# Kernel tuning notes

Measured on AMD Instinct MI355X. Metric: run time of the kernel, lower is better.

## Reference

```python
import jax, jax.numpy as jnp
import numpy as np

F_DIM = 64; HID = 256; P_ETA = 32; NBINS = 16; MULT = 3 * NBINS - 1
NLAYERS = 8; NBLOCKS = 2; TAIL = 10.0
MIN_BW = 1e-8; MIN_BH = 1e-8; MIN_D = 1e-8
THETA_DIM = F_DIM + 1
N_BATCH = 8192; M_DATA = 256


def _masks():
    in_deg = np.arange(1, F_DIM + 1)
    hid_deg = np.arange(HID) % (F_DIM - 1) + 1
    out_deg = np.repeat(in_deg, MULT)  # output index f*MULT+m has degree f+1
    m_in = (hid_deg[:, None] >= in_deg[None, :]).astype(np.float32)
    m_hh = (hid_deg[:, None] >= hid_deg[None, :]).astype(np.float32)
    m_out = (out_deg[:, None] > hid_deg[None, :]).astype(np.float32)
    return jnp.asarray(m_in), jnp.asarray(m_hh), jnp.asarray(m_out)


def _rqs_forward(x, uw, uh, ud):
    # unconstrained rational-quadratic spline with linear tails (nflows math)
    const = float(np.log(np.exp(1.0 - MIN_D) - 1.0))
    inside = (x >= -TAIL) & (x <= TAIL)
    ud = jnp.pad(ud, ((0, 0), (0, 0), (1, 1)), constant_values=const)  # [N,F,NBINS+1]
    w = jax.nn.softmax(uw, -1)
    w = MIN_BW + (1.0 - MIN_BW * NBINS) * w
    cw = jnp.concatenate([jnp.zeros_like(w[..., :1]), jnp.cumsum(w, -1)], -1)
    cw = 2.0 * TAIL * cw - TAIL
    cw = cw.at[..., 0].set(-TAIL).at[..., -1].set(TAIL)
    w = jnp.diff(cw, axis=-1)
    h = jax.nn.softmax(uh, -1)
    h = MIN_BH + (1.0 - MIN_BH * NBINS) * h
    ch = jnp.concatenate([jnp.zeros_like(h[..., :1]), jnp.cumsum(h, -1)], -1)
    ch = 2.0 * TAIL * ch - TAIL
    ch = ch.at[..., 0].set(-TAIL).at[..., -1].set(TAIL)
    h = jnp.diff(ch, axis=-1)
    d = MIN_D + jax.nn.softplus(ud)
    xs = jnp.clip(x, -TAIL, TAIL)
    idx = jnp.clip(jnp.sum((xs[..., None] >= cw).astype(jnp.int32), -1) - 1, 0, NBINS - 1)
    g = lambda a, i: jnp.take_along_axis(a, i[..., None], -1)[..., 0]
    icw, ich = g(cw, idx), g(ch, idx)
    iw, ih = g(w, idx), g(h, idx)
    delta = ih / iw
    d0, d1 = g(d, idx), g(d, idx + 1)
    t = (xs - icw) / iw
    tt = t * (1.0 - t)
    denom = delta + (d0 + d1 - 2.0 * delta) * tt
    y = ich + ih * (delta * t * t + d0 * tt) / denom
    dnum = delta * delta * (d1 * t * t + 2.0 * delta * tt + d0 * (1.0 - t) * (1.0 - t))
    ld = jnp.log(dnum) - 2.0 * jnp.log(denom)
    return jnp.where(inside, y, x), jnp.where(inside, ld, 0.0)


def _flow_transform(z, eta, W_in, b_in, W_ctx, b_ctx, W_blk, b_blk, W_out, b_out):
    m_in, m_hh, m_out = _masks()
    sqrt_h = jnp.sqrt(jnp.asarray(HID, z.dtype))

    def layer(carry, p):
        x, ld = carry
        Wi, bi, Wc, bc, Wb, bb, Wo, bo = p
        x = jnp.flip(x, axis=1)  # ReversePermutation (logdet 0)
        h = x @ (Wi * m_in).T + bi + eta @ Wc.T + bc  # MADE initial + context
        for k in range(NBLOCKS):  # masked pre-activation residual blocks
            t = jax.nn.relu(h)
            t = t @ (Wb[k, 0] * m_hh).T + bb[k, 0]
            t = jax.nn.relu(t)
            t = t @ (Wb[k, 1] * m_hh).T + bb[k, 1]
            h = h + t
        out = (h @ (Wo * m_out).T + bo).reshape(x.shape[0], F_DIM, MULT)
        uw = out[..., :NBINS] / sqrt_h
        uh = out[..., NBINS:2 * NBINS] / sqrt_h
        ud = out[..., 2 * NBINS:]
        x, l = _rqs_forward(x, uw, uh, ud)
        return (x, ld + l.sum(-1)), None

    init = (z, jnp.zeros(z.shape[0], z.dtype))
    (x, ld), _ = jax.lax.scan(layer, init, (W_in, b_in, W_ctx, b_ctx, W_blk, b_blk, W_out, b_out))
    return x, ld


def _stick_breaking(x):
    log_v = -jax.nn.softplus(-x)
    log_1v = -jax.nn.softplus(x)
    prefix = jnp.concatenate([jnp.zeros_like(x[:, :1]), jnp.cumsum(log_1v[:, :-1], 1)], 1)
    log_theta = jnp.concatenate([log_v + prefix, log_1v.sum(1, keepdims=True)], 1)
    wts = jnp.arange(F_DIM, 0, -1, dtype=x.dtype)
    log_det = log_v.sum(1) + (wts * log_1v).sum(1)
    return jnp.exp(log_theta), log_det


def setup_inputs() -> dict:
    key = jax.random.key(0)
    ks = jax.random.split(key, 8)
    s = 0.05
    return {
        'z': jax.random.normal(ks[0], (N_BATCH, F_DIM), jnp.float32),
        'eta_batch': jax.random.normal(ks[1], (N_BATCH, P_ETA), jnp.float32),
        'data_D2': jax.random.normal(ks[2], (M_DATA, THETA_DIM), jnp.float32),
        'W_in': s * jax.random.normal(ks[3], (NLAYERS, HID, F_DIM), jnp.float32),
        'b_in': jnp.zeros((NLAYERS, HID), jnp.float32),
        'W_ctx': s * jax.random.normal(ks[4], (NLAYERS, HID, P_ETA), jnp.float32),
        'b_ctx': jnp.zeros((NLAYERS, HID), jnp.float32),
        'W_blk': s * jax.random.normal(ks[5], (NLAYERS, NBLOCKS, 2, HID, HID), jnp.float32),
        'b_blk': jnp.zeros((NLAYERS, NBLOCKS, 2, HID), jnp.float32),
        'W_out': s * jax.random.normal(ks[6], (NLAYERS, F_DIM * MULT, HID), jnp.float32),
        'b_out': jnp.zeros((NLAYERS, F_DIM * MULT), jnp.float32),
    }


def reference(z, eta_batch, data_D2, W_in, b_in, W_ctx, b_ctx, W_blk, b_blk, W_out, b_out):
    x, flow_ld = _flow_transform(z, eta_batch, W_in, b_in, W_ctx, b_ctx, W_blk, b_blk, W_out, b_out)
    theta, sb_ld = _stick_breaking(x)
    total_ld = flow_ld + sb_ld
    log_qz = -0.5 * jnp.sum(z * z, -1) - 0.5 * F_DIM * jnp.log(2.0 * jnp.pi).astype(z.dtype)
    log_q = log_qz - total_ld
    # prior: Dirichlet(alpha=2) unnormalized: sum log(theta)
    log_p = jnp.sum(jnp.log(jnp.clip(theta, 1e-10, None)), -1)
    # likelihood: mean over data rows of isotropic Gaussian centered at theta
    d_sq = jnp.mean(jnp.sum(data_D2 * data_D2, -1))
    d_mean = jnp.mean(data_D2, 0)
    log_lik = -0.5 * (d_sq - 2.0 * theta @ d_mean + jnp.sum(theta * theta, -1))
    return jnp.mean(log_q - (log_p + log_lik))
```

## Files before the change

### kernel.cpp

```cpp
#include <hip/hip_runtime.h>
#include <hip/hip_fp8.h>
#include <math.h>

typedef float f32x4 __attribute__((ext_vector_type(4)));
typedef unsigned short u16;
typedef unsigned char u8;

typedef const __attribute__((address_space(1))) unsigned int ga_u32;
typedef __attribute__((address_space(3))) unsigned int ls_u32;

__device__ __forceinline__ void gl16(const void* g, void* l) {
    __builtin_amdgcn_global_load_lds((ga_u32*)g, (ls_u32*)l, 16, 0, 0);
}

__device__ __forceinline__ u16 f2bf(float f) {
    union { float f; unsigned u; } v; v.f = f;
    return (u16)((v.u + 0x7FFFu + ((v.u >> 16) & 1u)) >> 16);
}
__device__ __forceinline__ float bf2f(u16 h) {
    union { unsigned u; float f; } v; v.u = ((unsigned)h) << 16;
    return v.f;
}
__device__ __forceinline__ u8 f2q(float f) {
    __hip_fp8_e4m3 t(f);
    return (u8)t.__x;
}
__device__ __forceinline__ long ld8(const u8* p) { return *(const long*)p; }

__device__ __forceinline__ float splusf(float x) {
    return fmaxf(x, 0.f) + __logf(1.f + __expf(-fabsf(x)));
}
__device__ __forceinline__ int invperm(int k) {
    int m, q;
    if (k < 20) { m = k / 5; q = k - 5 * m; }
    else        { m = (k - 4) >> 2; q = (k - 4) & 3; }
    return m + 63 * q;
}

#define MID_ACT_P 272
#define WSCALE 64.f
#define WINV (1.f / 64.f)

__global__ __launch_bounds__(256) void setup_w(
    const float* __restrict__ Win, const float* __restrict__ bin,
    const float* __restrict__ Wctx, const float* __restrict__ bctx,
    const float* __restrict__ Wblk, const float* __restrict__ Wout,
    const float* __restrict__ bout, const float* __restrict__ eta,
    const float* __restrict__ z, const float* __restrict__ bblk,
    u8* __restrict__ W1, float* __restrict__ B1, u8* __restrict__ WB,
    u8* __restrict__ WO, float* __restrict__ BO, u8* __restrict__ AXE,
    float* __restrict__ XF, float* __restrict__ BBp)
{
    const long N1 = 8L * 8 * 8 * 64 * 8;
    const long N2 = 8L * 256;
    const long N3 = 8L * 4 * 8 * 9 * 64 * 8;
    const long N4 = 8L * 32 * 8 * 6 * 64 * 8;
    const long N5 = 8L * 3072;
    const long N6 = 8192L * 32;
    const long N7 = 8192L * 64;
    const long N8 = 8L * 4 * 256;
    const long tot = N1 + N2 + N3 + N4 + N5 + N6 + N7 + N8;
    for (long i = (long)blockIdx.x * blockDim.x + threadIdx.x; i < tot;
         i += (long)gridDim.x * blockDim.x) {
        long t = i;
        if (t < N1) {
            int off = (int)(t & 7), lane = (int)((t >> 3) & 63);
            int frag = (int)((t >> 9) & 7), wv = (int)((t >> 12) & 7);
            long l = t >> 15;
            int ks = frag >> 1, f = frag & 1;
            int pblk = f ? (15 - wv) : wv;
            int prow = pblk * 16 + (lane & 15);
            int row = invperm(prow);
            int c = ks * 32 + ((lane >> 4) << 3) + off;
            float v = 0.f;
            if (c < 64)      v = Win[(l * 256 + row) * 64 + c] * (((row % 63) >= c) ? 1.f : 0.f);
            else if (c < 96) v = Wctx[(l * 256 + row) * 32 + (c - 64)];
            W1[t] = f2q(v * WSCALE);
        } else if ((t -= N1) < N2) {
            long l = t >> 8; int k = (int)(t & 255);
            int c = invperm(k);
            B1[t] = bin[l * 256 + c] + bctx[l * 256 + c];
        } else if ((t -= N2) < N3) {
            int off = (int)(t & 7), lane = (int)((t >> 3) & 63);
            long r5 = t >> 9;
            int frag = (int)(r5 % 9); long r6 = r5 / 9;
            int wv = (int)(r6 & 7);
            int bi = (int)((r6 >> 3) & 3);
            long l = r6 >> 5;
            int kA = (wv + 2) >> 1;
            int pblk, ksl;
            if (frag < kA) { pblk = wv;      ksl = frag; }
            else           { pblk = 15 - wv; ksl = frag - kA; }
            int prow = pblk * 16 + (lane & 15);
            int pc   = ksl * 32 + ((lane >> 4) << 3) + off;
            int row = invperm(prow), c = invperm(pc);
            float v = Wblk[(((size_t)l * 4 + bi) * 256 + row) * 256 + c] *
                      (((row % 63) >= (c % 63)) ? 1.f : 0.f);
            WB[t] = f2q(v * WSCALE);
        } else if ((t -= N3) < N4) {
            long l = t / 786432; int rem = (int)(t % 786432);
            int y = rem / 24576, r2 = rem % 24576;
            int ks = r2 / 3072, r3 = r2 % 3072;
            int frag = r3 / 512, r4 = r3 % 512;
            int lane = r4 / 8, off = r4 % 8;
            int op = y * 96 + frag * 16 + (lane & 15);
            int pj = ks * 32 + ((lane >> 4) << 3) + off;
            int j = invperm(pj);
            int fd = op / 48, mm = op % 48;
            float v = 0.f;
            if (mm < 47 && fd > (j % 63))
                v = Wout[((size_t)l * 3008 + fd * 47 + mm) * 256 + j];
            WO[t] = f2q(v * WSCALE);
        } else if ((t -= N4) < N5) {
            long l = t / 3072; int op = (int)(t % 3072);
            int fd = op / 48, mm = op % 48;
            BO[t] = (mm < 47) ? bout[l * 3008 + (long)fd * 47 + mm] : 0.f;
        } else if ((t -= N5) < N6) {
            long b = t / 32; int p = (int)(t % 32);
            AXE[b * 96 + 64 + p] = f2q(eta[t]);
        } else if ((t -= N6) < N7) {
            long b = t >> 6; int f = (int)(t & 63);
            float v = z[b * 64 + (63 - f)];
            XF[t] = v;
            AXE[b * 96 + f] = f2q(v);
        } else {
            t -= N7;
            int k = (int)(t & 255);
            BBp[t] = bblk[(t & ~(long)255) | invperm(k)];
        }
    }
}

__global__ __launch_bounds__(128) void dstat(const float* __restrict__ D,
                                             float* __restrict__ DM)
{
    int j = threadIdx.x;
    float s = 0.f, q = 0.f;
    if (j < 65) {
        for (int m = 0; m < 256; ++m) {
            float v = D[m * 65 + j];
            s += v; q += v * v;
        }
        DM[j] = s * (1.f / 256.f);
    }
    __shared__ float red[128];
    red[j] = q; __syncthreads();
    for (int st = 64; st > 0; st >>= 1) {
        if (j < st) red[j] += red[j + st];
        __syncthreads();
    }
    if (j == 0) DM[65] = red[0] * (1.f / 256.f);
}

template<int KA>
__device__ __forceinline__ void wb_stage(
    const u8* __restrict__ gW, const u8* __restrict__ act,
    int lane, int fr, int kg, f32x4& T0, f32x4& T1)
{
    constexpr int KB = 9 - KA;
    long wf[9];
#pragma unroll
    for (int j = 0; j < 9; ++j)
        wf[j] = ld8(gW + (j * 64 + lane) * 8);
#pragma unroll
    for (int j = 0; j < KA; ++j) {
        long af = ld8(&act[fr * MID_ACT_P + j * 32 + kg * 8]);
        T0 = __builtin_amdgcn_mfma_f32_16x16x32_fp8_fp8(wf[j], af, T0, 0, 0, 0);
    }
#pragma unroll
    for (int j = 0; j < KB; ++j) {
        long af = ld8(&act[fr * MID_ACT_P + j * 32 + kg * 8]);
        T1 = __builtin_amdgcn_mfma_f32_16x16x32_fp8_fp8(wf[KA + j], af, T1, 0, 0, 0);
    }
}

__global__ __launch_bounds__(512) void fused_mid(
    const u8* __restrict__ AXE, const u8* __restrict__ W1l,
    const float* __restrict__ B1l, const u8* __restrict__ WBl,
    const float* __restrict__ bbl, u8* __restrict__ HB)
{
    __shared__ u8 act[2][16 * MID_ACT_P];
    const int tid = threadIdx.x;
    const int lane = tid & 63;
    const int wv = tid >> 6;
    const int fr = lane & 15, kg = lane >> 4;
    const int b0 = blockIdx.x * 16;
    const int cbA = wv * 16 + kg * 4;
    const int cbB = (15 - wv) * 16 + kg * 4;

    if (tid < 96) {
        int row = tid / 6, part = tid - row * 6;
        *(int4*)&act[0][row * MID_ACT_P + part * 16] =
            *(const int4*)&AXE[(size_t)(b0 + row) * 96 + part * 16];
    }

    f32x4 H0, H1, T0, T1;

    auto zeroT = [&]() {
        T0 = (f32x4){0.f, 0.f, 0.f, 0.f};
        T1 = (f32x4){0.f, 0.f, 0.f, 0.f};
    };
    auto epi1 = [&](f32x4& T, f32x4& H, int cb, const float* bias, int mode,
                    u8* actw) {
        const float4 bs = *(const float4*)&bias[cb];
        f32x4 v = T;
        v[0] = v[0] * WINV + bs.x; v[1] = v[1] * WINV + bs.y;
        v[2] = v[2] * WINV + bs.z; v[3] = v[3] * WINV + bs.w;
        if (mode == 0) H = v;
        if (mode == 2 || mode == 3) {
            H[0] += v[0]; H[1] += v[1]; H[2] += v[2]; H[3] += v[3];
            v = H;
        }
        unsigned pk;
        if (mode != 3) {
            pk = (unsigned)f2q(fmaxf(v[0], 0.f))
               | ((unsigned)f2q(fmaxf(v[1], 0.f)) << 8)
               | ((unsigned)f2q(fmaxf(v[2], 0.f)) << 16)
               | ((unsigned)f2q(fmaxf(v[3], 0.f)) << 24);
            *(unsigned*)&actw[fr * MID_ACT_P + cb] = pk;
        } else {
            pk = (unsigned)f2q(v[0]) | ((unsigned)f2q(v[1]) << 8)
               | ((unsigned)f2q(v[2]) << 16) | ((unsigned)f2q(v[3]) << 24);
            const int b = b0 + fr;
            const size_t idx =
                (((((size_t)(b >> 7) * 8 + (cb >> 5)) * 8 + ((b >> 4) & 7)) * 64)
                 + (((cb >> 3) & 3) * 16 + (b & 15))) * 8 + (cb & 7);
            *(unsigned*)&HB[idx] = pk;
        }
    };
    auto epi = [&](const float* bias, int mode, u8* actw) {
        epi1(T0, H0, cbA, bias, mode, actw);
        epi1(T1, H1, cbB, bias, mode, actw);
    };
    auto wbrun = [&](const u8* gW, const u8* actr) {
        switch (wv >> 1) {
        case 0: wb_stage<1>(gW, actr, lane, fr, kg, T0, T1); break;
        case 1: wb_stage<2>(gW, actr, lane, fr, kg, T0, T1); break;
        case 2: wb_stage<3>(gW, actr, lane, fr, kg, T0, T1); break;
        default: wb_stage<4>(gW, actr, lane, fr, kg, T0, T1); break;
        }
    };

    zeroT();
    {
        const u8* gW = W1l + wv * 4096;
        long wf[6];
#pragma unroll
        for (int j = 0; j < 6; ++j)
            wf[j] = ld8(gW + (j * 64 + lane) * 8);
        __syncthreads();
#pragma unroll
        for (int ks = 0; ks < 3; ++ks) {
            long af = ld8(&act[0][fr * MID_ACT_P + ks * 32 + kg * 8]);
            T0 = __builtin_amdgcn_mfma_f32_16x16x32_fp8_fp8(wf[ks * 2 + 0], af, T0, 0, 0, 0);
            T1 = __builtin_amdgcn_mfma_f32_16x16x32_fp8_fp8(wf[ks * 2 + 1], af, T1, 0, 0, 0);
        }
    }
    epi(B1l, 0, act[1]);
    zeroT();
    __syncthreads();
    wbrun(WBl + 0 * 36864 + wv * 4608, act[1]);
    epi(bbl, 1, act[0]);
    zeroT();
    __syncthreads();
    wbrun(WBl + 1 * 36864 + wv * 4608, act[0]);
    epi(bbl + 256, 2, act[1]);
    zeroT();
    __syncthreads();
    wbrun(WBl + 2 * 36864 + wv * 4608, act[1]);
    epi(bbl + 2 * 256, 1, act[0]);
    zeroT();
    __syncthreads();
    wbrun(WBl + 3 * 36864 + wv * 4608, act[0]);
    epi(bbl + 3 * 256, 3, (u8*)nullptr);
}

__global__ __launch_bounds__(256) void gemm_out_spline(
    const u8* __restrict__ A, const u8* __restrict__ Wo,
    const float* __restrict__ bo, const float* __restrict__ XF,
    float* __restrict__ Xn, float* __restrict__ XFnext, u8* __restrict__ AXE,
    float* __restrict__ LDP, int first)
{
    __shared__ u16 SM16[13312];
    u8* SM8 = (u8*)SM16;
    const int tid = threadIdx.x;
    const int lane = tid & 63, wv = tid >> 6;
    const int wm = wv >> 1, wn = wv & 1;
    const int fr = lane & 15, kg = lane >> 4;
    const int by = 31 - (int)blockIdx.y;
    const int m0 = blockIdx.x * 128, n0 = by * 96;
    const int nk = (by + 4) >> 2;

    u8* Ab = SM8;
    u8* Bb = SM8 + 8192;

    const u8* gA = A  + (size_t)blockIdx.x * 16384;
    const u8* gB = Wo + (size_t)by * 24576;

    f32x4 acc[4][3];
#pragma unroll
    for (int m = 0; m < 4; ++m)
#pragma unroll
        for (int n = 0; n < 3; ++n) acc[m][n] = (f32x4){0.f, 0.f, 0.f, 0.f};

    gl16(gA + tid * 16, Ab + tid * 16);
    if (tid < 192) gl16(gB + tid * 16, Bb + tid * 16);

    for (int ks = 0; ks < nk; ++ks) {
        __syncthreads();
        if (ks + 1 < nk) {
            const u8* sa = gA + (ks + 1) * 4096;
            const u8* sb = gB + (ks + 1) * 3072;
            u8* na = Ab + ((ks + 1) & 1) * 4096;
            u8* nb = Bb + ((ks + 1) & 1) * 3072;
            gl16(sa + tid * 16, na + tid * 16);
            if (tid < 192) gl16(sb + tid * 16, nb + tid * 16);
        }
        const u8* cA = Ab + (ks & 1) * 4096;
        const u8* cB = Bb + (ks & 1) * 3072;
        long af[4], bf[3];
#pragma unroll
        for (int m = 0; m < 4; ++m)
            af[m] = ld8(&cA[(wm * 4 + m) * 512 + lane * 8]);
#pragma unroll
        for (int n = 0; n < 3; ++n)
            bf[n] = ld8(&cB[(wn * 3 + n) * 512 + lane * 8]);
#pragma unroll
        for (int m = 0; m < 4; ++m)
#pragma unroll
            for (int n = 0; n < 3; ++n)
                acc[m][n] = __builtin_amdgcn_mfma_f32_16x16x32_fp8_fp8(bf[n], af[m], acc[m][n], 0, 0, 0);
    }
    __syncthreads();

#pragma unroll
    for (int m = 0; m < 4; ++m) {
        const int row = wm * 64 + m * 16 + fr;
#pragma unroll
        for (int n = 0; n < 3; ++n) {
            const int c0 = wn * 48 + n * 16 + kg * 4;
            const float4 bs = *(const float4*)&bo[n0 + c0];
            short4 q;
            q.x = (short)f2bf(acc[m][n][0] * WINV + bs.x);
            q.y = (short)f2bf(acc[m][n][1] * WINV + bs.y);
            q.z = (short)f2bf(acc[m][n][2] * WINV + bs.z);
            q.w = (short)f2bf(acc[m][n][3] * WINV + bs.w);
            *(short4*)&SM16[row * 104 + c0] = q;
        }
    }
    __syncthreads();

    typedef short bf16x8 __attribute__((ext_vector_type(8)));
    const int r = tid >> 1, fi = tid & 1;
    const int b = m0 + r;
    const int fg = by * 2 + fi;
    const u16* o_ = &SM16[r * 104 + fi * 48];
    bf16x8 v0 = *(const bf16x8*)(o_);
    bf16x8 v1 = *(const bf16x8*)(o_ + 8);
    bf16x8 v2 = *(const bf16x8*)(o_ + 16);
    bf16x8 v3 = *(const bf16x8*)(o_ + 24);
    bf16x8 v4 = *(const bf16x8*)(o_ + 32);
    bf16x8 v5 = *(const bf16x8*)(o_ + 40);

    float xin = XF[(size_t)b * 64 + fg];
    bool inside = (xin >= -10.f) && (xin <= 10.f);
    float xs = fminf(fmaxf(xin, -10.f), 10.f);

    float ew[16], eh[16], ud[15];
#pragma unroll
    for (int i = 0; i < 8; ++i) {
        ew[i]     = bf2f((u16)v0[i]) * 0.0625f;
        ew[8 + i] = bf2f((u16)v1[i]) * 0.0625f;
        eh[i]     = bf2f((u16)v2[i]) * 0.0625f;
        eh[8 + i] = bf2f((u16)v3[i]) * 0.0625f;
    }
#pragma unroll
    for (int i = 0; i < 8; ++i) ud[i] = bf2f((u16)v4[i]);
#pragma unroll
    for (int i = 0; i < 7; ++i) ud[8 + i] = bf2f((u16)v5[i]);

    float mw = ew[0], mh = eh[0];
#pragma unroll
    for (int i = 1; i < 16; ++i) { mw = fmaxf(mw, ew[i]); mh = fmaxf(mh, eh[i]); }
    float sw = 0.f, sh = 0.f;
#pragma unroll
    for (int i = 0; i < 16; ++i) {
        ew[i] = __expf(ew[i] - mw); sw += ew[i];
        eh[i] = __expf(eh[i] - mh); sh += eh[i];
    }
    const float kw = 20.f * (1.f - 1.6e-7f) / sw;
    const float kh = 20.f * (1.f - 1.6e-7f) / sh;

    float cwk = -10.f, chk = -10.f;
    float icw = -10.f, ich = -10.f, iw = 1.f, ih = 1.f, udl = 0.f, udr = 0.f;
    int selk = 0;
#pragma unroll
    for (int k = 0; k < 16; ++k) {
        const float cw1 = (k == 15) ? 10.f : cwk + (2e-7f + kw * ew[k]);
        const float ch1 = (k == 15) ? 10.f : chk + (2e-7f + kh * eh[k]);
        if (xs >= cwk) {
            selk = k;
            icw = cwk; iw = cw1 - cwk;
            ich = chk; ih = ch1 - chk;
            udl = (k >= 1)  ? ud[k - 1] : 0.f;
            udr = (k <= 14) ? ud[k]     : 0.f;
        }
        cwk = cw1; chk = ch1;
    }
    float d0 = (selk == 0)  ? 1.f : 1e-8f + splusf(udl);
    float d1 = (selk == 15) ? 1.f : 1e-8f + splusf(udr);
    float delta = ih / iw;
    float t = (xs - icw) / iw;
    float tt = t * (1.f - t);
    float denom = delta + (d0 + d1 - 2.f * delta) * tt;
    float y = ich + ih * (delta * t * t + d0 * tt) / denom;
    float omt = 1.f - t;
    float dnum = delta * delta * (d1 * t * t + 2.f * delta * tt + d0 * omt * omt);
    float ldv = __logf(dnum) - 2.f * __logf(denom);
    if (!inside) { y = xin; ldv = 0.f; }

    Xn[(size_t)b * 64 + fg] = y;
    XFnext[(size_t)b * 64 + (63 - fg)] = y;
    AXE[(size_t)b * 96 + (63 - fg)] = f2q(y);

    float other = __shfl_xor(ldv, 1);
    if (fi == 0) {
        size_t o = (size_t)b * 32 + by;
        float v = ldv + other;
        LDP[o] = first ? v : (LDP[o] + v);
    }
}

__global__ __launch_bounds__(256) void final1(
    const float* __restrict__ X, const float* __restrict__ z,
    const float* __restrict__ LDP, const float* __restrict__ DM,
    float* __restrict__ PART)
{
    int tid = threadIdx.x;
    int b = blockIdx.x * 256 + tid;
    float ldt = 0.f;
    for (int g = 0; g < 32; ++g) ldt += LDP[(size_t)b * 32 + g];
    float pre = 0.f, lvs = 0.f, wls = 0.f, lp = 0.f, tdm = 0.f, tsq = 0.f;
    const float LCLIP = -23.02585093f;
    for (int i = 0; i < 64; ++i) {
        float xi = X[(size_t)b * 64 + i];
        float lv = -splusf(-xi), l1 = -splusf(xi);
        float lt = lv + pre;
        float th = __expf(lt);
        lp += fmaxf(lt, LCLIP);
        tdm += th * DM[i]; tsq += th * th;
        lvs += lv; wls += (float)(64 - i) * l1;
        pre += l1;
    }
    float th = __expf(pre);
    lp += fmaxf(pre, LCLIP); tdm += th * DM[64]; tsq += th * th;
    float zs = 0.f;
    for (int i = 0; i < 64; ++i) { float zz = z[(size_t)b * 64 + i]; zs += zz * zz; }
    float logqz = -0.5f * zs - 58.812066f;
    float log_q = logqz - (ldt + lvs + wls);
    float log_lik = -0.5f * (DM[65] - 2.f * tdm + tsq);
    float val = log_q - lp - log_lik;

    __shared__ float red[256];
    red[tid] = val; __syncthreads();
    for (int s = 128; s > 0; s >>= 1) {
        if (tid < s) red[tid] += red[tid + s];
        __syncthreads();
    }
    if (tid == 0) PART[blockIdx.x] = red[0];
}

__global__ __launch_bounds__(64) void final2(const float* __restrict__ PART,
                                             float* __restrict__ out)
{
    int tid = threadIdx.x;
    float s = (tid < 32) ? PART[tid] : 0.f;
    for (int o = 16; o > 0; o >>= 1) s += __shfl_down(s, o);
    if (tid == 0) out[0] = s * (1.f / 8192.f);
}

extern "C" void kernel_launch(void* const* d_in, const int* in_sizes, int n_in,
                              void* d_out, int out_size, void* d_ws, size_t ws_size,
                              hipStream_t stream)
{
    (void)in_sizes; (void)n_in; (void)out_size; (void)ws_size;
    const float* z    = (const float*)d_in[0];
    const float* eta  = (const float*)d_in[1];
    const float* dat  = (const float*)d_in[2];
    const float* Win  = (const float*)d_in[3];
    const float* bin  = (const float*)d_in[4];
    const float* Wctx = (const float*)d_in[5];
    const float* bctx = (const float*)d_in[6];
    const float* Wblk = (const float*)d_in[7];
    const float* bblk = (const float*)d_in[8];
    const float* Wout = (const float*)d_in[9];
    const float* bout = (const float*)d_in[10];
    float* out = (float*)d_out;

    char* w = (char*)d_ws;
    size_t off = 0;
    auto alloc = [&](size_t bytes) {
        void* p = w + off;
        off += (bytes + 255) & ~(size_t)255;
        return p;
    };
    u8*    W1  = (u8*)   alloc(8L * 32768);
    float* B1  = (float*)alloc(8L * 256 * 4);
    u8*    WB  = (u8*)   alloc(8L * 147456);
    float* BBp = (float*)alloc(8L * 4 * 256 * 4);
    u8*    WO  = (u8*)   alloc(8L * 786432);
    float* BO  = (float*)alloc(8L * 3072 * 4);
    u8*    AXE = (u8*)   alloc(8192L * 96);
    float* XFa = (float*)alloc(8192L * 64 * 4);
    float* XFb = (float*)alloc(8192L * 64 * 4);
    float* XC  = (float*)alloc(8192L * 64 * 4);
    u8*    HB  = (u8*)   alloc(8192L * 256);
    float* LDP = (float*)alloc(8192L * 32 * 4);
    float* DM  = (float*)alloc(66 * 4);
    float* PART= (float*)alloc(64 * 4);

    setup_w<<<dim3(2048), dim3(256), 0, stream>>>(
        Win, bin, Wctx, bctx, Wblk, Wout, bout, eta, z, bblk,
        W1, B1, WB, WO, BO, AXE, XFa, BBp);
    dstat<<<dim3(1), dim3(128), 0, stream>>>(dat, DM);

    for (int l = 0; l < 8; ++l) {
        float* XFin  = (l & 1) ? XFb : XFa;
        float* XFout = (l & 1) ? XFa : XFb;
        fused_mid<<<dim3(512), dim3(512), 0, stream>>>(
            AXE, W1 + (size_t)l * 32768, B1 + l * 256,
            WB + (size_t)l * 147456, BBp + (size_t)l * 4 * 256, HB);
        gemm_out_spline<<<dim3(64, 32), dim3(256), 0, stream>>>(
            HB, WO + (size_t)l * 786432, BO + l * 3072, XFin,
            XC, XFout, AXE, LDP, (l == 0) ? 1 : 0);
    }
    final1<<<dim3(32), dim3(256), 0, stream>>>(XC, z, LDP, DM, PART);
    final2<<<dim3(1), dim3(64), 0, stream>>>(PART, out);
}
```

Measured before the change: 282.6 us.

## Pair complementary output tiles per block and fold data stats into final kernel

The output GEMM+spline kernel now runs half as many blocks, each processing two column tiles (by=31-p and by=p) whose K-depths are complementary, balancing the triangular MADE workload across blocks and reusing the A tile region. Separately, the single-block data-statistics kernel is removed and each final1 block recomputes the data means in shared memory, saving one launch at the cost of redundant reads of the small data matrix. Pairing reduces grid parallelism to 1024 blocks and serializes two tiles within each block.

```diff
diff --git a/kernel.cpp b/kernel.cpp
--- a/kernel.cpp
+++ b/kernel.cpp
@@ -131,27 +131,6 @@
     }
 }
 
-__global__ __launch_bounds__(128) void dstat(const float* __restrict__ D,
-                                             float* __restrict__ DM)
-{
-    int j = threadIdx.x;
-    float s = 0.f, q = 0.f;
-    if (j < 65) {
-        for (int m = 0; m < 256; ++m) {
-            float v = D[m * 65 + j];
-            s += v; q += v * v;
-        }
-        DM[j] = s * (1.f / 256.f);
-    }
-    __shared__ float red[128];
-    red[j] = q; __syncthreads();
-    for (int st = 64; st > 0; st >>= 1) {
-        if (j < st) red[j] += red[j + st];
-        __syncthreads();
-    }
-    if (j == 0) DM[65] = red[0] * (1.f / 256.f);
-}
-
 template<int KA>
 __device__ __forceinline__ void wb_stage(
     const u8* __restrict__ gW, const u8* __restrict__ act,
@@ -287,156 +266,185 @@
     const int lane = tid & 63, wv = tid >> 6;
     const int wm = wv >> 1, wn = wv & 1;
     const int fr = lane & 15, kg = lane >> 4;
-    const int by = 31 - (int)blockIdx.y;
-    const int m0 = blockIdx.x * 128, n0 = by * 96;
-    const int nk = (by + 4) >> 2;
+    const int p = (int)blockIdx.y;
+    const int m0 = blockIdx.x * 128;
 
     u8* Ab = SM8;
     u8* Bb = SM8 + 8192;
-
-    const u8* gA = A  + (size_t)blockIdx.x * 16384;
-    const u8* gB = Wo + (size_t)by * 24576;
-
-    f32x4 acc[4][3];
-#pragma unroll
-    for (int m = 0; m < 4; ++m)
-#pragma unroll
-        for (int n = 0; n < 3; ++n) acc[m][n] = (f32x4){0.f, 0.f, 0.f, 0.f};
-
-    gl16(gA + tid * 16, Ab + tid * 16);
-    if (tid < 192) gl16(gB + tid * 16, Bb + tid * 16);
-
-    for (int ks = 0; ks < nk; ++ks) {
+    const u8* gA = A + (size_t)blockIdx.x * 16384;
+
+    typedef short bf16x8 __attribute__((ext_vector_type(8)));
+
+#pragma unroll
+    for (int half = 0; half < 2; ++half) {
+        const int by = half ? p : (31 - p);
+        const int n0 = by * 96;
+        const int nk = (by + 4) >> 2;
+        const u8* gB = Wo + (size_t)by * 24576;
+
+        f32x4 acc[4][3];
+#pragma unroll
+        for (int m = 0; m < 4; ++m)
+#pragma unroll
+            for (int n = 0; n < 3; ++n) acc[m][n] = (f32x4){0.f, 0.f, 0.f, 0.f};
+
+        if (half) __syncthreads();
+
+        gl16(gA + tid * 16, Ab + tid * 16);
+        if (tid < 192) gl16(gB + tid * 16, Bb + tid * 16);
+
+        for (int ks = 0; ks < nk; ++ks) {
+            __syncthreads();
+            if (ks + 1 < nk) {
+                const u8* sa = gA + (ks + 1) * 4096;
+                const u8* sb = gB + (ks + 1) * 3072;
+                u8* na = Ab + ((ks + 1) & 1) * 4096;
+                u8* nb = Bb + ((ks + 1) & 1) * 3072;
+                gl16(sa + tid * 16, na + tid * 16);
+                if (tid < 192) gl16(sb + tid * 16, nb + tid * 16);
+            }
+            const u8* cA = Ab + (ks & 1) * 4096;
+            const u8* cB = Bb + (ks & 1) * 3072;
+            long af[4], bf[3];
+#pragma unroll
+            for (int m = 0; m < 4; ++m)
+                af[m] = ld8(&cA[(wm * 4 + m) * 512 + lane * 8]);
+#pragma unroll
+            for (int n = 0; n < 3; ++n)
+                bf[n] = ld8(&cB[(wn * 3 + n) * 512 + lane * 8]);
+#pragma unroll
+            for (int m = 0; m < 4; ++m)
+#pragma unroll
+                for (int n = 0; n < 3; ++n)
+                    acc[m][n] = __builtin_amdgcn_mfma_f32_16x16x32_fp8_fp8(bf[n], af[m], acc[m][n], 0, 0, 0);
+        }
         __syncthreads();
-        if (ks + 1 < nk) {
-            const u8* sa = gA + (ks + 1) * 4096;
-            const u8* sb = gB + (ks + 1) * 3072;
-            u8* na = Ab + ((ks + 1) & 1) * 4096;
-            u8* nb = Bb + ((ks + 1) & 1) * 3072;
-            gl16(sa + tid * 16, na + tid * 16);
-            if (tid < 192) gl16(sb + tid * 16, nb + tid * 16);
-        }
-        const u8* cA = Ab + (ks & 1) * 4096;
-        const u8* cB = Bb + (ks & 1) * 3072;
-        long af[4], bf[3];
-#pragma unroll
-        for (int m = 0; m < 4; ++m)
-            af[m] = ld8(&cA[(wm * 4 + m) * 512 + lane * 8]);
-#pragma unroll
-        for (int n = 0; n < 3; ++n)
-            bf[n] = ld8(&cB[(wn * 3 + n) * 512 + lane * 8]);
-#pragma unroll
-        for (int m = 0; m < 4; ++m)
-#pragma unroll
-            for (int n = 0; n < 3; ++n)
-                acc[m][n] = __builtin_amdgcn_mfma_f32_16x16x32_fp8_fp8(bf[n], af[m], acc[m][n], 0, 0, 0);
-    }
-    __syncthreads();
-
-#pragma unroll
-    for (int m = 0; m < 4; ++m) {
-        const int row = wm * 64 + m * 16 + fr;
-#pragma unroll
-        for (int n = 0; n < 3; ++n) {
-            const int c0 = wn * 48 + n * 16 + kg * 4;
-            const float4 bs = *(const float4*)&bo[n0 + c0];
-            short4 q;
-            q.x = (short)f2bf(acc[m][n][0] * WINV + bs.x);
-            q.y = (short)f2bf(acc[m][n][1] * WINV + bs.y);
-            q.z = (short)f2bf(acc[m][n][2] * WINV + bs.z);
-            q.w = (short)f2bf(acc[m][n][3] * WINV + bs.w);
-            *(short4*)&SM16[row * 104 + c0] = q;
-        }
-    }
-    __syncthreads();
-
-    typedef short bf16x8 __attribute__((ext_vector_type(8)));
-    const int r = tid >> 1, fi = tid & 1;
-    const int b = m0 + r;
-    const int fg = by * 2 + fi;
-    const u16* o_ = &SM16[r * 104 + fi * 48];
-    bf16x8 v0 = *(const bf16x8*)(o_);
-    bf16x8 v1 = *(const bf16x8*)(o_ + 8);
-    bf16x8 v2 = *(const bf16x8*)(o_ + 16);
-    bf16x8 v3 = *(const bf16x8*)(o_ + 24);
-    bf16x8 v4 = *(const bf16x8*)(o_ + 32);
-    bf16x8 v5 = *(const bf16x8*)(o_ + 40);
-
-    float xin = XF[(size_t)b * 64 + fg];
-    bool inside = (xin >= -10.f) && (xin <= 10.f);
-    float xs = fminf(fmaxf(xin, -10.f), 10.f);
-
-    float ew[16], eh[16], ud[15];
-#pragma unroll
-    for (int i = 0; i < 8; ++i) {
-        ew[i]     = bf2f((u16)v0[i]) * 0.0625f;
-        ew[8 + i] = bf2f((u16)v1[i]) * 0.0625f;
-        eh[i]     = bf2f((u16)v2[i]) * 0.0625f;
-        eh[8 + i] = bf2f((u16)v3[i]) * 0.0625f;
-    }
-#pragma unroll
-    for (int i = 0; i < 8; ++i) ud[i] = bf2f((u16)v4[i]);
-#pragma unroll
-    for (int i = 0; i < 7; ++i) ud[8 + i] = bf2f((u16)v5[i]);
-
-    float mw = ew[0], mh = eh[0];
-#pragma unroll
-    for (int i = 1; i < 16; ++i) { mw = fmaxf(mw, ew[i]); mh = fmaxf(mh, eh[i]); }
-    float sw = 0.f, sh = 0.f;
-#pragma unroll
-    for (int i = 0; i < 16; ++i) {
-        ew[i] = __expf(ew[i] - mw); sw += ew[i];
-        eh[i] = __expf(eh[i] - mh); sh += eh[i];
-    }
-    const float kw = 20.f * (1.f - 1.6e-7f) / sw;
-    const float kh = 20.f * (1.f - 1.6e-7f) / sh;
-
-    float cwk = -10.f, chk = -10.f;
-    float icw = -10.f, ich = -10.f, iw = 1.f, ih = 1.f, udl = 0.f, udr = 0.f;
-    int selk = 0;
-#pragma unroll
-    for (int k = 0; k < 16; ++k) {
-        const float cw1 = (k == 15) ? 10.f : cwk + (2e-7f + kw * ew[k]);
-        const float ch1 = (k == 15) ? 10.f : chk + (2e-7f + kh * eh[k]);
-        if (xs >= cwk) {
-            selk = k;
-            icw = cwk; iw = cw1 - cwk;
-            ich = chk; ih = ch1 - chk;
-            udl = (k >= 1)  ? ud[k - 1] : 0.f;
-            udr = (k <= 14) ? ud[k]     : 0.f;
-        }
-        cwk = cw1; chk = ch1;
-    }
-    float d0 = (selk == 0)  ? 1.f : 1e-8f + splusf(udl);
-    float d1 = (selk == 15) ? 1.f : 1e-8f + splusf(udr);
-    float delta = ih / iw;
-    float t = (xs - icw) / iw;
-    float tt = t * (1.f - t);
-    float denom = delta + (d0 + d1 - 2.f * delta) * tt;
-    float y = ich + ih * (delta * t * t + d0 * tt) / denom;
-    float omt = 1.f - t;
-    float dnum = delta * delta * (d1 * t * t + 2.f * delta * tt + d0 * omt * omt);
-    float ldv = __logf(dnum) - 2.f * __logf(denom);
-    if (!inside) { y = xin; ldv = 0.f; }
-
-    Xn[(size_t)b * 64 + fg] = y;
-    XFnext[(size_t)b * 64 + (63 - fg)] = y;
-    AXE[(size_t)b * 96 + (63 - fg)] = f2q(y);
-
-    float other = __shfl_xor(ldv, 1);
-    if (fi == 0) {
-        size_t o = (size_t)b * 32 + by;
-        float v = ldv + other;
-        LDP[o] = first ? v : (LDP[o] + v);
+
+#pragma unroll
+        for (int m = 0; m < 4; ++m) {
+            const int row = wm * 64 + m * 16 + fr;
+#pragma unroll
+            for (int n = 0; n < 3; ++n) {
+                const int c0 = wn * 48 + n * 16 + kg * 4;
+                const float4 bs = *(const float4*)&bo[n0 + c0];
+                short4 q;
+                q.x = (short)f2bf(acc[m][n][0] * WINV + bs.x);
+                q.y = (short)f2bf(acc[m][n][1] * WINV + bs.y);
+                q.z = (short)f2bf(acc[m][n][2] * WINV + bs.z);
+                q.w = (short)f2bf(acc[m][n][3] * WINV + bs.w);
+                *(short4*)&SM16[row * 104 + c0] = q;
+            }
+        }
+        __syncthreads();
+
+        const int r = tid >> 1, fi = tid & 1;
+        const int b = m0 + r;
+        const int fg = by * 2 + fi;
+        const u16* o_ = &SM16[r * 104 + fi * 48];
+        bf16x8 v0 = *(const bf16x8*)(o_);
+        bf16x8 v1 = *(const bf16x8*)(o_ + 8);
+        bf16x8 v2 = *(const bf16x8*)(o_ + 16);
+        bf16x8 v3 = *(const bf16x8*)(o_ + 24);
+        bf16x8 v4 = *(const bf16x8*)(o_ + 32);
+        bf16x8 v5 = *(const bf16x8*)(o_ + 40);
+
+        float xin = XF[(size_t)b * 64 + fg];
+        bool inside = (xin >= -10.f) && (xin <= 10.f);
+        float xs = fminf(fmaxf(xin, -10.f), 10.f);
+
+        float ew[16], eh[16], ud[15];
+#pragma unroll
+        for (int i = 0; i < 8; ++i) {
+            ew[i]     = bf2f((u16)v0[i]) * 0.0625f;
+            ew[8 + i] = bf2f((u16)v1[i]) * 0.0625f;
+            eh[i]     = bf2f((u16)v2[i]) * 0.0625f;
+            eh[8 + i] = bf2f((u16)v3[i]) * 0.0625f;
+        }
+#pragma unroll
+        for (int i = 0; i < 8; ++i) ud[i] = bf2f((u16)v4[i]);
+#pragma unroll
+        for (int i = 0; i < 7; ++i) ud[8 + i] = bf2f((u16)v5[i]);
+
+        float mw = ew[0], mh = eh[0];
+#pragma unroll
+        for (int i = 1; i < 16; ++i) { mw = fmaxf(mw, ew[i]); mh = fmaxf(mh, eh[i]); }
+        float sw = 0.f, sh = 0.f;
+#pragma unroll
+        for (int i = 0; i < 16; ++i) {
+            ew[i] = __expf(ew[i] - mw); sw += ew[i];
+            eh[i] = __expf(eh[i] - mh); sh += eh[i];
+        }
+        const float kw = 20.f * (1.f - 1.6e-7f) / sw;
+        const float kh = 20.f * (1.f - 1.6e-7f) / sh;
+
+        float cwk = -10.f, chk = -10.f;
+        float icw = -10.f, ich = -10.f, iw = 1.f, ih = 1.f, udl = 0.f, udr = 0.f;
+        int selk = 0;
+#pragma unroll
+        for (int k = 0; k < 16; ++k) {
+            const float cw1 = (k == 15) ? 10.f : cwk + (2e-7f + kw * ew[k]);
+            const float ch1 = (k == 15) ? 10.f : chk + (2e-7f + kh * eh[k]);
+            if (xs >= cwk) {
+                selk = k;
+                icw = cwk; iw = cw1 - cwk;
+                ich = chk; ih = ch1 - chk;
+                udl = (k >= 1)  ? ud[k - 1] : 0.f;
+                udr = (k <= 14) ? ud[k]     : 0.f;
+            }
+            cwk = cw1; chk = ch1;
+        }
+        float d0 = (selk == 0)  ? 1.f : 1e-8f + splusf(udl);
+        float d1 = (selk == 15) ? 1.f : 1e-8f + splusf(udr);
+        float delta = ih / iw;
+        float t = (xs - icw) / iw;
+        float tt = t * (1.f - t);
+        float denom = delta + (d0 + d1 - 2.f * delta) * tt;
+        float y = ich + ih * (delta * t * t + d0 * tt) / denom;
+        float omt = 1.f - t;
+        float dnum = delta * delta * (d1 * t * t + 2.f * delta * tt + d0 * omt * omt);
+        float ldv = __logf(dnum) - 2.f * __logf(denom);
+        if (!inside) { y = xin; ldv = 0.f; }
+
+        Xn[(size_t)b * 64 + fg] = y;
+        XFnext[(size_t)b * 64 + (63 - fg)] = y;
+        AXE[(size_t)b * 96 + (63 - fg)] = f2q(y);
+
+        float other = __shfl_xor(ldv, 1);
+        if (fi == 0) {
+            size_t o = (size_t)b * 32 + by;
+            float v = ldv + other;
+            LDP[o] = first ? v : (LDP[o] + v);
+        }
     }
 }
 
 __global__ __launch_bounds__(256) void final1(
     const float* __restrict__ X, const float* __restrict__ z,
-    const float* __restrict__ LDP, const float* __restrict__ DM,
+    const float* __restrict__ LDP, const float* __restrict__ D,
     float* __restrict__ PART)
 {
+    __shared__ float DMs[66];
+    __shared__ float red[256];
     int tid = threadIdx.x;
+
+    float q = 0.f;
+    if (tid < 65) {
+        float s = 0.f;
+        for (int m = 0; m < 256; ++m) {
+            float v = D[m * 65 + tid];
+            s += v; q += v * v;
+        }
+        DMs[tid] = s * (1.f / 256.f);
+    }
+    red[tid] = (tid < 65) ? q : 0.f;
+    __syncthreads();
+    for (int s = 128; s > 0; s >>= 1) {
+        if (tid < s) red[tid] += red[tid + s];
+        __syncthreads();
+    }
+    if (tid == 0) DMs[65] = red[0] * (1.f / 256.f);
+    __syncthreads();
+
     int b = blockIdx.x * 256 + tid;
     float ldt = 0.f;
     for (int g = 0; g < 32; ++g) ldt += LDP[(size_t)b * 32 + g];
@@ -448,20 +456,20 @@
         float lt = lv + pre;
         float th = __expf(lt);
         lp += fmaxf(lt, LCLIP);
-        tdm += th * DM[i]; tsq += th * th;
+        tdm += th * DMs[i]; tsq += th * th;
         lvs += lv; wls += (float)(64 - i) * l1;
         pre += l1;
     }
     float th = __expf(pre);
-    lp += fmaxf(pre, LCLIP); tdm += th * DM[64]; tsq += th * th;
+    lp += fmaxf(pre, LCLIP); tdm += th * DMs[64]; tsq += th * th;
     float zs = 0.f;
     for (int i = 0; i < 64; ++i) { float zz = z[(size_t)b * 64 + i]; zs += zz * zz; }
     float logqz = -0.5f * zs - 58.812066f;
     float log_q = logqz - (ldt + lvs + wls);
-    float log_lik = -0.5f * (DM[65] - 2.f * tdm + tsq);
+    float log_lik = -0.5f * (DMs[65] - 2.f * tdm + tsq);
     float val = log_q - lp - log_lik;
 
-    __shared__ float red[256];
+    __syncthreads();
     red[tid] = val; __syncthreads();
     for (int s = 128; s > 0; s >>= 1) {
         if (tid < s) red[tid] += red[tid + s];
@@ -516,13 +524,11 @@
     float* XC  = (float*)alloc(8192L * 64 * 4);
     u8*    HB  = (u8*)   alloc(8192L * 256);
     float* LDP = (float*)alloc(8192L * 32 * 4);
-    float* DM  = (float*)alloc(66 * 4);
     float* PART= (float*)alloc(64 * 4);
 
     setup_w<<<dim3(2048), dim3(256), 0, stream>>>(
         Win, bin, Wctx, bctx, Wblk, Wout, bout, eta, z, bblk,
         W1, B1, WB, WO, BO, AXE, XFa, BBp);
-    dstat<<<dim3(1), dim3(128), 0, stream>>>(dat, DM);
 
     for (int l = 0; l < 8; ++l) {
         float* XFin  = (l & 1) ? XFb : XFa;
@@ -530,10 +536,10 @@
         fused_mid<<<dim3(512), dim3(512), 0, stream>>>(
             AXE, W1 + (size_t)l * 32768, B1 + l * 256,
             WB + (size_t)l * 147456, BBp + (size_t)l * 4 * 256, HB);
-        gemm_out_spline<<<dim3(64, 32), dim3(256), 0, stream>>>(
+        gemm_out_spline<<<dim3(64, 16), dim3(256), 0, stream>>>(
             HB, WO + (size_t)l * 786432, BO + l * 3072, XFin,
             XC, XFout, AXE, LDP, (l == 0) ? 1 : 0);
     }
-    final1<<<dim3(32), dim3(256), 0, stream>>>(XC, z, LDP, DM, PART);
+    final1<<<dim3(32), dim3(256), 0, stream>>>(XC, z, LDP, dat, PART);
     final2<<<dim3(1), dim3(64), 0, stream>>>(PART, out);
 }
```

Result: slower. 298.1 us (+5.5%).
